# Performance work log

Hardware: AMD Instinct MI355X
Metric: run time of the kernel (lower is better)

Reference implementation:

```python
import jax, jax.numpy as jnp
import numpy as np

WIN_LEN = 5
RES_LEN = None


def _log_sparse_mask(Q_L, K_L, win_len=0, res_len=None):
    # Faithful port of LogSparseMask (numpy, static shapes -> constant-folded under jit)
    if res_len is None:
        L_ls = K_L - 1 - win_len
        n_reps = 1
    else:
        n_reps = int(np.ceil(K_L / res_len))
        L_ls = res_len
    l_floor = int(np.log2(L_ls))
    indxs = np.array([int(2 ** (l_floor - i)) for i in range(l_floor + 1)])
    reps_array = np.expand_dims(np.arange(n_reps, dtype='int') * L_ls, 1)
    indxs = (indxs + reps_array + win_len).flatten()
    indxs = indxs[indxs < K_L - 1]
    my_mask = np.ones(K_L, dtype='int')
    my_mask[indxs] = 0
    my_mask[:win_len + 1] = 0
    my_mask = np.concatenate([np.flip(my_mask[1:]), my_mask])
    my_mask = np.array([my_mask[K_L - i:K_L * 2 - i] for i in range(1, Q_L + 1)], dtype=bool)
    return my_mask  # [Q_L, K_L], True = masked out


def _combined_mask(L, S):
    causal = np.triu(np.ones((L, S), dtype=bool), k=1)  # TriangularCausalMask
    sparse = _log_sparse_mask(L, S, WIN_LEN, RES_LEN)
    return jnp.asarray(causal | sparse)[None, None]  # [1,1,L,S], broadcasts over B,H


def setup_inputs() -> dict:
    key = jax.random.key(0)
    k1, k2, k3 = jax.random.split(key, 3)
    B, L, H, E, D = 4, 2048, 8, 64, 64
    return {
        'queries': jax.random.normal(k1, (B, L, H, E), dtype=jnp.float32),
        'keys': jax.random.normal(k2, (B, L, H, E), dtype=jnp.float32),
        'values': jax.random.normal(k3, (B, L, H, D), dtype=jnp.float32),
    }


def reference(queries, keys, values):
    B, L, H, E = queries.shape
    S = keys.shape[1]
    scale = 1.0 / np.sqrt(E)  # self.scale is None -> 1/sqrt(E)
    # [B,H,L,S] full score matrix (eager), then causal|log-sparse masked_fill(-inf)
    scores = jnp.einsum('blhe,bshe->bhls', queries, keys)
    mask = _combined_mask(L, S)
    scores = jnp.where(mask, -jnp.inf, scale * scores)
    A = jax.nn.softmax(scores, axis=-1)  # dropout p=0.0 (eval) -> identity
    V = jnp.einsum('bhls,bshd->blhd', A, values)
    return V  # module returns (V, None); attention weights not output
```

## Files before the change

### kernel.cpp

```cpp
#include <hip/hip_runtime.h>
#include <stdint.h>


static constexpr int Bn = 4, Ln = 2048, Hn = 8, En = 64;
static constexpr int NDELTA = 17;

__global__ __launch_bounds__(256) void logsparse_attn_kernel(
    const float* __restrict__ Q,
    const float* __restrict__ K,
    const float* __restrict__ V,
    float* __restrict__ O)
{
    constexpr int deltas[NDELTA] = {0,1,2,3,4,5,6,7,9,13,21,37,69,133,261,517,1029};

    const int bh = blockIdx.x & 31;
    const int l  = blockIdx.x >> 5;
    const int b  = bh >> 3;
    const int h  = bh & 7;

    const int sub = threadIdx.x & 7;
    const int q   = l * 32 + (threadIdx.x >> 3);

    const size_t bhBase = ((size_t)b * Ln * Hn + (size_t)h) * (size_t)En;
    const size_t rowQ   = bhBase + (size_t)q * (Hn * En);
    const int    dimOff = sub * 8;

    const float4 q0 = *(const float4*)(Q + rowQ + dimOff);
    const float4 q1 = *(const float4*)(Q + rowQ + dimOff + 4);
    float qf[8] = { q0.x*0.125f, q0.y*0.125f, q0.z*0.125f, q0.w*0.125f,
                    q1.x*0.125f, q1.y*0.125f, q1.z*0.125f, q1.w*0.125f };

    float sc[NDELTA];
    #pragma unroll
    for (int d = 0; d < NDELTA; ++d) {
        const int j  = q - deltas[d];
        const int jc = (j < 0) ? 0 : j;
        const float* kp = K + bhBase + (size_t)jc * (Hn * En) + dimOff;
        const float4 k0 = *(const float4*)(kp);
        const float4 k1 = *(const float4*)(kp + 4);
        float s = qf[0]*k0.x + qf[1]*k0.y + qf[2]*k0.z + qf[3]*k0.w
                + qf[4]*k1.x + qf[5]*k1.y + qf[6]*k1.z + qf[7]*k1.w;
        s += __shfl_xor(s, 1);
        s += __shfl_xor(s, 2);
        s += __shfl_xor(s, 4);
        sc[d] = (j < 0) ? -__builtin_inff() : s;
    }

    float m = sc[0];
    #pragma unroll
    for (int d = 1; d < NDELTA; ++d) m = fmaxf(m, sc[d]);
    float p[NDELTA];
    float sum = 0.0f;
    #pragma unroll
    for (int d = 0; d < NDELTA; ++d) {
        p[d] = __expf(sc[d] - m);
        sum += p[d];
    }
    const float inv = 1.0f / sum;

    float acc[8] = {0,0,0,0,0,0,0,0};
    #pragma unroll
    for (int d = 0; d < NDELTA; ++d) {
        const int j  = q - deltas[d];
        const int jc = (j < 0) ? 0 : j;
        const float* vp = V + bhBase + (size_t)jc * (Hn * En) + dimOff;
        const float4 v0 = *(const float4*)(vp);
        const float4 v1 = *(const float4*)(vp + 4);
        const float w = p[d];
        acc[0] = fmaf(w, v0.x, acc[0]);
        acc[1] = fmaf(w, v0.y, acc[1]);
        acc[2] = fmaf(w, v0.z, acc[2]);
        acc[3] = fmaf(w, v0.w, acc[3]);
        acc[4] = fmaf(w, v1.x, acc[4]);
        acc[5] = fmaf(w, v1.y, acc[5]);
        acc[6] = fmaf(w, v1.z, acc[6]);
        acc[7] = fmaf(w, v1.w, acc[7]);
    }

    float4 o0, o1;
    o0.x = acc[0]*inv; o0.y = acc[1]*inv; o0.z = acc[2]*inv; o0.w = acc[3]*inv;
    o1.x = acc[4]*inv; o1.y = acc[5]*inv; o1.z = acc[6]*inv; o1.w = acc[7]*inv;
    *(float4*)(O + rowQ + dimOff)     = o0;
    *(float4*)(O + rowQ + dimOff + 4) = o1;
}

extern "C" void kernel_launch(void* const* d_in, const int* in_sizes, int n_in,
                              void* d_out, int out_size, void* d_ws, size_t ws_size,
                              hipStream_t stream) {
    const float* Q = (const float*)d_in[0];
    const float* K = (const float*)d_in[1];
    const float* V = (const float*)d_in[2];
    float* O = (float*)d_out;

    const int total_threads = Bn * Hn * Ln * 8;
    logsparse_attn_kernel<<<total_threads / 256, 256, 0, stream>>>(Q, K, V, O);
}
```

Before: 107.7 us.

## Stage nearby K/V rows in shared memory for the dense window deltas

Each block of 32 queries cooperatively loads the 69 K and V rows it needs for the small offsets (delta up to 37) into padded shared memory. Those deltas are then read from LDS, while the far offsets still come from global memory. The aim is to cut redundant global and L2 traffic, since neighbouring queries touch overlapping rows. In exchange it adds a barrier, about 37KB of shared memory per block, and some staged rows that go unused, which may lower occupancy.

```diff
diff --git a/kernel.cpp b/kernel.cpp
--- a/kernel.cpp
+++ b/kernel.cpp
@@ -4,6 +4,9 @@
 
 static constexpr int Bn = 4, Ln = 2048, Hn = 8, En = 64;
 static constexpr int NDELTA = 17;
+static constexpr int NEAR_MAX = 37;
+static constexpr int SPAN = 69;
+static constexpr int PADF = 68;
 
 __global__ __launch_bounds__(256) void logsparse_attn_kernel(
     const float* __restrict__ Q,
@@ -13,31 +16,59 @@
 {
     constexpr int deltas[NDELTA] = {0,1,2,3,4,5,6,7,9,13,21,37,69,133,261,517,1029};
 
+    __shared__ float Ks[SPAN * PADF];
+    __shared__ float Vs[SPAN * PADF];
+
     const int bh = blockIdx.x & 31;
     const int l  = blockIdx.x >> 5;
     const int b  = bh >> 3;
     const int h  = bh & 7;
+    const int q0 = l * 32;
 
-    const int sub = threadIdx.x & 7;
-    const int q   = l * 32 + (threadIdx.x >> 3);
+    const int tid = threadIdx.x;
+    const size_t bhBase = ((size_t)b * Ln * Hn + (size_t)h) * (size_t)En;
+    constexpr int ROWF = Hn * En;
 
-    const size_t bhBase = ((size_t)b * Ln * Hn + (size_t)h) * (size_t)En;
-    const size_t rowQ   = bhBase + (size_t)q * (Hn * En);
-    const int    dimOff = sub * 8;
+    for (int idx = tid; idx < 2 * SPAN * 16; idx += 256) {
+        const int ten = (idx >= SPAN * 16);
+        const int rem = ten ? idx - SPAN * 16 : idx;
+        const int rid = rem >> 4;
+        const int ch  = rem & 15;
+        int g = q0 - NEAR_MAX + rid;
+        if (g < 0) g = 0;
+        const float* src = (ten ? V : K) + bhBase + (size_t)g * ROWF + ch * 4;
+        float* dst = (ten ? Vs : Ks) + rid * PADF + ch * 4;
+        *(float4*)dst = *(const float4*)src;
+    }
+    __syncthreads();
 
-    const float4 q0 = *(const float4*)(Q + rowQ + dimOff);
-    const float4 q1 = *(const float4*)(Q + rowQ + dimOff + 4);
-    float qf[8] = { q0.x*0.125f, q0.y*0.125f, q0.z*0.125f, q0.w*0.125f,
-                    q1.x*0.125f, q1.y*0.125f, q1.z*0.125f, q1.w*0.125f };
+    const int sub = tid & 7;
+    const int qq  = tid >> 3;
+    const int q   = q0 + qq;
+    const int dimOff = sub * 8;
+    const size_t rowQ = bhBase + (size_t)q * ROWF;
+
+    const float4 q0v = *(const float4*)(Q + rowQ + dimOff);
+    const float4 q1v = *(const float4*)(Q + rowQ + dimOff + 4);
+    const float qf[8] = { q0v.x*0.125f, q0v.y*0.125f, q0v.z*0.125f, q0v.w*0.125f,
+                          q1v.x*0.125f, q1v.y*0.125f, q1v.z*0.125f, q1v.w*0.125f };
 
     float sc[NDELTA];
     #pragma unroll
     for (int d = 0; d < NDELTA; ++d) {
-        const int j  = q - deltas[d];
-        const int jc = (j < 0) ? 0 : j;
-        const float* kp = K + bhBase + (size_t)jc * (Hn * En) + dimOff;
-        const float4 k0 = *(const float4*)(kp);
-        const float4 k1 = *(const float4*)(kp + 4);
+        const int del = deltas[d];
+        const int j   = q - del;
+        float4 k0, k1;
+        if (del <= NEAR_MAX) {
+            const float* kp = Ks + (qq + NEAR_MAX - del) * PADF + dimOff;
+            k0 = *(const float4*)(kp);
+            k1 = *(const float4*)(kp + 4);
+        } else {
+            const int jc = (j < 0) ? 0 : j;
+            const float* kp = K + bhBase + (size_t)jc * ROWF + dimOff;
+            k0 = *(const float4*)(kp);
+            k1 = *(const float4*)(kp + 4);
+        }
         float s = qf[0]*k0.x + qf[1]*k0.y + qf[2]*k0.z + qf[3]*k0.w
                 + qf[4]*k1.x + qf[5]*k1.y + qf[6]*k1.z + qf[7]*k1.w;
         s += __shfl_xor(s, 1);
@@ -61,11 +92,19 @@
     float acc[8] = {0,0,0,0,0,0,0,0};
     #pragma unroll
     for (int d = 0; d < NDELTA; ++d) {
-        const int j  = q - deltas[d];
-        const int jc = (j < 0) ? 0 : j;
-        const float* vp = V + bhBase + (size_t)jc * (Hn * En) + dimOff;
-        const float4 v0 = *(const float4*)(vp);
-        const float4 v1 = *(const float4*)(vp + 4);
+        const int del = deltas[d];
+        const int j   = q - del;
+        float4 v0, v1;
+        if (del <= NEAR_MAX) {
+            const float* vp = Vs + (qq + NEAR_MAX - del) * PADF + dimOff;
+            v0 = *(const float4*)(vp);
+            v1 = *(const float4*)(vp + 4);
+        } else {
+            const int jc = (j < 0) ? 0 : j;
+            const float* vp = V + bhBase + (size_t)jc * ROWF + dimOff;
+            v0 = *(const float4*)(vp);
+            v1 = *(const float4*)(vp + 4);
+        }
         const float w = p[d];
         acc[0] = fmaf(w, v0.x, acc[0]);
         acc[1] = fmaf(w, v0.y, acc[1]);
@@ -92,6 +131,6 @@
     const float* V = (const float*)d_in[2];
     float* O = (float*)d_out;
 
-    const int total_threads = Bn * Hn * Ln * 8;
-    logsparse_attn_kernel<<<total_threads / 256, 256, 0, stream>>>(Q, K, V, O);
+    const int nblocks = Bn * Hn * (Ln / 32);
+    logsparse_attn_kernel<<<nblocks, 256, 0, stream>>>(Q, K, V, O);
 }
```

Result: faster. 102.1 us (-5.2%).
